# Kernel tuning notes

Hardware: AMD Instinct MI355X
Metric: run time of the kernel (lower is better)

Reference implementation:

```python
import jax, jax.numpy as jnp
import numpy as np

EPS = 1e-05
B, I, N, O = 1024, 256, 1024, 256

def setup_inputs() -> dict:
    key = jax.random.key(0)
    ks = jax.random.split(key, 6)
    return {
        "x_re": jax.random.normal(ks[0], (B, I, 1), dtype=jnp.float32),
        "x_im": jax.random.normal(ks[1], (B, I, 1), dtype=jnp.float32),
        "G_re": jax.random.normal(ks[2], (I, N), dtype=jnp.float32) / np.sqrt(I).astype(np.float32),
        "G_im": jax.random.normal(ks[3], (I, N), dtype=jnp.float32) / np.sqrt(I).astype(np.float32),
        "s_re": jnp.ones((1, N), dtype=jnp.float32),
        "s_im": jnp.ones((1, N), dtype=jnp.float32),
        "W_re": jax.random.normal(ks[4], (N, O), dtype=jnp.float32) * np.float32(np.sqrt(5 * np.exp(2) * I / (12 * N * O))),
        "W_im": jax.random.normal(ks[5], (N, O), dtype=jnp.float32) * np.float32(np.sqrt(5 * np.exp(2) * I / (12 * N * O))),
        "b_re": jnp.zeros((1, O), dtype=jnp.float32),
        "b_im": jnp.zeros((1, O), dtype=jnp.float32),
    }

def reference(x_re, x_im, G_re, G_im, s_re, s_im, W_re, W_im, b_re, b_im):
    # (B, inputs, 1) - (inputs, neurons) -> (B, inputs, neurons); reduce over inputs
    v_re = jnp.sum((x_re - G_re) ** 2, axis=1, keepdims=True)  # (B, 1, N)
    v_im = jnp.sum((x_im - G_im) ** 2, axis=1, keepdims=True)  # (B, 1, N)
    phi_re = jnp.exp(-v_re / jnp.maximum(s_re, EPS))  # (B, 1, N)
    phi_im = jnp.exp(-v_im / jnp.maximum(s_im, EPS))  # (B, 1, N)
    # complex matmul (phi_re + i phi_im) @ (W_re + i W_im) + (b_re + i b_im)
    y_re = jnp.matmul(phi_re, W_re) - jnp.matmul(phi_im, W_im) + b_re  # (B, 1, O)
    y_im = jnp.matmul(phi_re, W_im) + jnp.matmul(phi_im, W_re) + b_im  # (B, 1, O)
    return jnp.stack([y_re, y_im], axis=-1)  # (B, 1, O, 2) = real/imag
```

## Files before the change

### kernel.cpp

```cpp
#include <hip/hip_runtime.h>
#include <math.h>

#define B_ 1024
#define I_ 256
#define N_ 1024
#define O_ 256
#define EPSV 1e-5f

typedef unsigned short u16;
typedef short bf16x8 __attribute__((ext_vector_type(8)));
typedef float f32x4 __attribute__((ext_vector_type(4)));
typedef int i32x4 __attribute__((ext_vector_type(4)));

__device__ inline u16 f2bf(float f) {
    union { float f; unsigned int u; } v; v.f = f;
    unsigned int r = v.u + 0x7FFFu + ((v.u >> 16) & 1u);
    return (u16)(r >> 16);
}


__device__ inline void transconv_frag(const float* __restrict__ in,
                                      u16* __restrict__ out, int R, int C,
                                      int r0, int c0, int t, float (*tile)[69],
                                      float* __restrict__ gpart) {
    const int lr = t >> 2, lq = t & 3;
    #pragma unroll
    for (int j = 0; j < 4; ++j) {
        float4 v = *(const float4*)(in + (size_t)(r0 + lr) * C + c0 + lq * 16 + j * 4);
        *(float4*)&tile[lr][lq * 16 + j * 4] = v;
    }
    __syncthreads();
    const int oc = t >> 2, oq = t & 3;
    const int row = c0 + oc;
    const int ktiles = R >> 5;
    float ss = 0.f;
    #pragma unroll
    for (int h = 0; h < 2; ++h) {
        const int k0 = r0 + oq * 16 + h * 8;
        const int kt = k0 >> 5, quad = (k0 >> 3) & 3;
        __align__(16) u16 tmp[8];
        #pragma unroll
        for (int e = 0; e < 8; ++e) {
            const float g = tile[oq * 16 + h * 8 + e][oc];
            ss += g * g;
            tmp[e] = f2bf(g);
        }
        const size_t off = ((size_t)((row >> 4) * ktiles + kt)) * 512
                         + (quad * 16 + (row & 15)) * 8;
        *(int4*)(out + off) = *(const int4*)tmp;
    }
    if (gpart) {
        ss += __shfl_xor(ss, 1);
        ss += __shfl_xor(ss, 2);
        if (oq == 0) gpart[(r0 >> 6) * C + row] = ss;
    }
}

__global__ __launch_bounds__(256) void prep_kernel(
    const float* __restrict__ x_re, const float* __restrict__ x_im,
    const float* __restrict__ G_re, const float* __restrict__ G_im,
    const float* __restrict__ W_re, const float* __restrict__ W_im,
    u16* __restrict__ Xfr, u16* __restrict__ Xfi,
    u16* __restrict__ GTfr, u16* __restrict__ GTfi,
    u16* __restrict__ WTfr, u16* __restrict__ WTfi,
    float* __restrict__ xsq_re, float* __restrict__ xsq_im,
    float* __restrict__ gsq_re_part, float* __restrict__ gsq_im_part)
{
    __shared__ float smem[64][69];
    const int blk = blockIdx.x, t = threadIdx.x;

    if (blk < 32) {
        const int unit = blk * 4 + (t >> 6);
        const int comp = unit >> 6, mt = unit & 63;
        const int lane = t & 63;
        const int l16 = lane & 15, quad = lane >> 4;
        const float* src = (comp ? x_im : x_re)
                         + (size_t)(mt * 16 + l16) * I_ + quad * 8;
        u16* dstbase = (comp ? Xfi : Xfr) + (size_t)(mt * 8) * 512 + lane * 8;
        float ssum = 0.f;
        #pragma unroll
        for (int kt = 0; kt < 8; ++kt) {
            float4 a0 = *(const float4*)(src + kt * 32);
            float4 a1 = *(const float4*)(src + kt * 32 + 4);
            ssum += a0.x*a0.x + a0.y*a0.y + a0.z*a0.z + a0.w*a0.w
                  + a1.x*a1.x + a1.y*a1.y + a1.z*a1.z + a1.w*a1.w;
            __align__(16) u16 tmp[8];
            tmp[0] = f2bf(a0.x); tmp[1] = f2bf(a0.y);
            tmp[2] = f2bf(a0.z); tmp[3] = f2bf(a0.w);
            tmp[4] = f2bf(a1.x); tmp[5] = f2bf(a1.y);
            tmp[6] = f2bf(a1.z); tmp[7] = f2bf(a1.w);
            *(int4*)(dstbase + (size_t)kt * 512) = *(const int4*)tmp;
        }
        ssum += __shfl_xor(ssum, 16);
        ssum += __shfl_xor(ssum, 32);
        if (lane < 16) {
            float* xsq = comp ? xsq_im : xsq_re;
            xsq[mt * 16 + lane] = ssum;
        }
    } else if (blk < 160) {
        const int local = blk - 32;
        const int comp = local >> 6, rem = local & 63;
        const int rt = rem >> 4, ct = rem & 15;
        transconv_frag(comp ? G_im : G_re, comp ? GTfi : GTfr,
                       I_, N_, rt * 64, ct * 64, t, smem,
                       comp ? gsq_im_part : gsq_re_part);
    } else {
        const int local = blk - 160;
        const int comp = local >> 6, rem = local & 63;
        const int rt = rem >> 2, ct = rem & 3;
        transconv_frag(comp ? W_im : W_re, comp ? WTfi : WTfr,
                       N_, O_, rt * 64, ct * 64, t, smem, (float*)0);
    }
}

__global__ __launch_bounds__(256) void phi_mfma(
    const u16* __restrict__ Xfr, const u16* __restrict__ Xfi,
    const u16* __restrict__ GTfr, const u16* __restrict__ GTfi,
    const float* __restrict__ xsq_re, const float* __restrict__ xsq_im,
    const float* __restrict__ gsq_re_part, const float* __restrict__ gsq_im_part,
    const float* __restrict__ s_re, const float* __restrict__ s_im,
    u16* __restrict__ Pfr, u16* __restrict__ Pfi)
{
    __shared__ u16 pbuf[8 * 512];
    const int z = blockIdx.z;
    const u16* Xf  = z ? Xfi : Xfr;
    const u16* GTf = z ? GTfi : GTfr;
    const float* xsq = z ? xsq_im : xsq_re;
    const float* gp  = z ? gsq_im_part : gsq_re_part;
    const float* s   = z ? s_im : s_re;
    u16* Pf = z ? Pfi : Pfr;

    const int t = threadIdx.x;
    const int w = t >> 6, lane = t & 63;
    const int quad = lane >> 4, l16 = lane & 15;
    const int mw = (w >> 1) * 32, nw = (w & 1) * 32;
    const int mt0 = blockIdx.y * 4 + (mw >> 4);
    const int nt0 = blockIdx.x * 4 + (nw >> 4);

    const u16* Ab = Xf  + lane * 8;
    const u16* Bb = GTf + lane * 8;
    const size_t a0o = (size_t)(mt0 * 8) * 512;
    const size_t a1o = (size_t)((mt0 + 1) * 8) * 512;
    const size_t b0o = (size_t)(nt0 * 8) * 512;
    const size_t b1o = (size_t)((nt0 + 1) * 8) * 512;

    bf16x8 cA0 = *(const bf16x8*)(Ab + a0o);
    bf16x8 cA1 = *(const bf16x8*)(Ab + a1o);
    bf16x8 cB0 = *(const bf16x8*)(Bb + b0o);
    bf16x8 cB1 = *(const bf16x8*)(Bb + b1o);

    f32x4 acc[2][2] = {};
    #pragma unroll
    for (int kt = 0; kt < 8; ++kt) {
        bf16x8 nA0, nA1, nB0, nB1;
        if (kt < 7) {
            const size_t ko = (size_t)(kt + 1) * 512;
            nA0 = *(const bf16x8*)(Ab + a0o + ko);
            nA1 = *(const bf16x8*)(Ab + a1o + ko);
            nB0 = *(const bf16x8*)(Bb + b0o + ko);
            nB1 = *(const bf16x8*)(Bb + b1o + ko);
        }
        acc[0][0] = __builtin_amdgcn_mfma_f32_16x16x32_bf16(cA0, cB0, acc[0][0], 0, 0, 0);
        acc[0][1] = __builtin_amdgcn_mfma_f32_16x16x32_bf16(cA0, cB1, acc[0][1], 0, 0, 0);
        acc[1][0] = __builtin_amdgcn_mfma_f32_16x16x32_bf16(cA1, cB0, acc[1][0], 0, 0, 0);
        acc[1][1] = __builtin_amdgcn_mfma_f32_16x16x32_bf16(cA1, cB1, acc[1][1], 0, 0, 0);
        cA0 = nA0; cA1 = nA1; cB0 = nB0; cB1 = nB1;
    }

    const int m0 = blockIdx.y * 64, n0 = blockIdx.x * 64;
    #pragma unroll
    for (int mt = 0; mt < 2; ++mt)
        #pragma unroll
        for (int nt = 0; nt < 2; ++nt) {
            const int col = nw + nt * 16 + l16;
            const int gn = n0 + col;
            const float gq = gp[gn] + gp[N_ + gn] + gp[2 * N_ + gn] + gp[3 * N_ + gn];
            const float inv_s = 1.0f / fmaxf(s[gn], EPSV);
            #pragma unroll
            for (int r = 0; r < 4; ++r) {
                const int row = mw + mt * 16 + quad * 4 + r;
                const float v = xsq[m0 + row] - 2.0f * acc[mt][nt][r] + gq;
                const u16 p = f2bf(__expf(-v * inv_s));
                const int lt = (row >> 4) * 2 + (col >> 5);
                pbuf[lt * 512 + (((col >> 3) & 3) * 16 + (row & 15)) * 8 + (col & 7)] = p;
            }
        }
    __syncthreads();

    const int lt = t >> 5, s32 = t & 31;
    const int mt_g = blockIdx.y * 4 + (lt >> 1);
    const int kt_g = blockIdx.x * 2 + (lt & 1);
    const u16* src = pbuf + lt * 512 + s32 * 16;
    u16* dst = Pf + (size_t)(mt_g * 32 + kt_g) * 512 + s32 * 16;
    *(int4*)dst = *(const int4*)src;
    *((int4*)dst + 1) = *((const int4*)src + 1);
}

__global__ __launch_bounds__(256) void y_mfma(
    const u16* __restrict__ Pfr, const u16* __restrict__ Pfi,
    const u16* __restrict__ WTfr, const u16* __restrict__ WTfi,
    const float* __restrict__ b_re, const float* __restrict__ b_im,
    float* __restrict__ out)
{
    __shared__ float red[4][2][16][34];
    const int t = threadIdx.x;
    const int w = t >> 6, lane = t & 63;
    const int quad = lane >> 4, l16 = lane & 15;
    const int pm = blockIdx.y;
    const int wo0 = blockIdx.x * 2;

    const u16* Ar = Pfr + lane * 8;
    const u16* Ai = Pfi + lane * 8;
    const u16* Br = WTfr + lane * 8;
    const u16* Bi = WTfi + lane * 8;
    const size_t ao = (size_t)(pm * 32 + w * 8) * 512;
    const size_t b0o = (size_t)(wo0 * 32 + w * 8) * 512;
    const size_t b1o = (size_t)((wo0 + 1) * 32 + w * 8) * 512;

    bf16x8 cAr = *(const bf16x8*)(Ar + ao);
    bf16x8 cAi = *(const bf16x8*)(Ai + ao);
    bf16x8 cBr0 = *(const bf16x8*)(Br + b0o);
    bf16x8 cBi0 = *(const bf16x8*)(Bi + b0o);
    bf16x8 cBr1 = *(const bf16x8*)(Br + b1o);
    bf16x8 cBi1 = *(const bf16x8*)(Bi + b1o);

    f32x4 cr[2] = {}, ci[2] = {};
    #pragma unroll
    for (int ks = 0; ks < 8; ++ks) {
        bf16x8 nAr, nAi, nBr0, nBi0, nBr1, nBi1;
        if (ks < 7) {
            const size_t ko = (size_t)(ks + 1) * 512;
            nAr  = *(const bf16x8*)(Ar + ao + ko);
            nAi  = *(const bf16x8*)(Ai + ao + ko);
            nBr0 = *(const bf16x8*)(Br + b0o + ko);
            nBi0 = *(const bf16x8*)(Bi + b0o + ko);
            nBr1 = *(const bf16x8*)(Br + b1o + ko);
            nBi1 = *(const bf16x8*)(Bi + b1o + ko);
        }
        i32x4 tv = (*(const i32x4*)&cAi) ^ 0x80008000;
        bf16x8 cAn = *(const bf16x8*)&tv;
        cr[0] = __builtin_amdgcn_mfma_f32_16x16x32_bf16(cAr, cBr0, cr[0], 0, 0, 0);
        cr[0] = __builtin_amdgcn_mfma_f32_16x16x32_bf16(cAn, cBi0, cr[0], 0, 0, 0);
        ci[0] = __builtin_amdgcn_mfma_f32_16x16x32_bf16(cAr, cBi0, ci[0], 0, 0, 0);
        ci[0] = __builtin_amdgcn_mfma_f32_16x16x32_bf16(cAi, cBr0, ci[0], 0, 0, 0);
        cr[1] = __builtin_amdgcn_mfma_f32_16x16x32_bf16(cAr, cBr1, cr[1], 0, 0, 0);
        cr[1] = __builtin_amdgcn_mfma_f32_16x16x32_bf16(cAn, cBi1, cr[1], 0, 0, 0);
        ci[1] = __builtin_amdgcn_mfma_f32_16x16x32_bf16(cAr, cBi1, ci[1], 0, 0, 0);
        ci[1] = __builtin_amdgcn_mfma_f32_16x16x32_bf16(cAi, cBr1, ci[1], 0, 0, 0);
        cAr = nAr; cAi = nAi;
        cBr0 = nBr0; cBi0 = nBi0; cBr1 = nBr1; cBi1 = nBi1;
    }

    #pragma unroll
    for (int nt = 0; nt < 2; ++nt) {
        const int o = nt * 16 + l16;
        #pragma unroll
        for (int r = 0; r < 4; ++r) {
            const int b = quad * 4 + r;
            red[w][0][b][o] = cr[nt][r];
            red[w][1][b][o] = ci[nt][r];
        }
    }
    __syncthreads();

    const int b = t >> 4, oq = t & 15;
    const int o = oq * 2;
    const int gb = blockIdx.y * 16 + b;
    const int go = blockIdx.x * 32 + o;
    float r0 = red[0][0][b][o]   + red[1][0][b][o]   + red[2][0][b][o]   + red[3][0][b][o];
    float i0 = red[0][1][b][o]   + red[1][1][b][o]   + red[2][1][b][o]   + red[3][1][b][o];
    float r1 = red[0][0][b][o+1] + red[1][0][b][o+1] + red[2][0][b][o+1] + red[3][0][b][o+1];
    float i1 = red[0][1][b][o+1] + red[1][1][b][o+1] + red[2][1][b][o+1] + red[3][1][b][o+1];
    float4 v;
    v.x = r0 + b_re[go];     v.y = i0 + b_im[go];
    v.z = r1 + b_re[go + 1]; v.w = i1 + b_im[go + 1];
    *(float4*)(out + ((size_t)gb * O_ + go) * 2) = v;
}

extern "C" void kernel_launch(void* const* d_in, const int* in_sizes, int n_in,
                              void* d_out, int out_size, void* d_ws, size_t ws_size,
                              hipStream_t stream) {
    const float* x_re = (const float*)d_in[0];
    const float* x_im = (const float*)d_in[1];
    const float* G_re = (const float*)d_in[2];
    const float* G_im = (const float*)d_in[3];
    const float* s_re = (const float*)d_in[4];
    const float* s_im = (const float*)d_in[5];
    const float* W_re = (const float*)d_in[6];
    const float* W_im = (const float*)d_in[7];
    const float* b_re = (const float*)d_in[8];
    const float* b_im = (const float*)d_in[9];
    float* out = (float*)d_out;

    u16* Xfr  = (u16*)d_ws;
    u16* Xfi  = Xfr  + (size_t)B_ * I_;
    u16* GTfr = Xfi  + (size_t)B_ * I_;
    u16* GTfi = GTfr + (size_t)N_ * I_;
    u16* WTfr = GTfi + (size_t)N_ * I_;
    u16* WTfi = WTfr + (size_t)O_ * N_;
    u16* Pfr  = WTfi + (size_t)O_ * N_;
    u16* Pfi  = Pfr  + (size_t)B_ * N_;
    float* xsq_re = (float*)(Pfi + (size_t)B_ * N_);
    float* xsq_im = xsq_re + B_;
    float* gsq_re_part = xsq_im + B_;
    float* gsq_im_part = gsq_re_part + 4 * N_;

    prep_kernel<<<288, 256, 0, stream>>>(
        x_re, x_im, G_re, G_im, W_re, W_im,
        Xfr, Xfi, GTfr, GTfi, WTfr, WTfi,
        xsq_re, xsq_im, gsq_re_part, gsq_im_part);

    phi_mfma<<<dim3(N_ / 64, B_ / 64, 2), 256, 0, stream>>>(
        Xfr, Xfi, GTfr, GTfi, xsq_re, xsq_im, gsq_re_part, gsq_im_part,
        s_re, s_im, Pfr, Pfi);

    y_mfma<<<dim3(O_ / 32, B_ / 16), 256, 0, stream>>>(
        Pfr, Pfi, WTfr, WTfi, b_re, b_im, out);
}
```

Baseline: 91.26 us.

## Fuse prep conversion into phi kernel, converting X and G on the fly

Removes the separate prep kernel. The phi kernel now loads fp32 X directly, converts it to bf16 in registers with packed convert instructions, and computes row norms inline. Each block transposes and converts its 64-column G slice into LDS fragments and computes the G norms locally. An extra column of blocks converts W for the y kernel. This saves one launch and the workspace round-trip, but each G slice is now redundantly converted by all 16 row-blocks, and fp32 X is reread per column block.

```diff
diff --git a/kernel.cpp b/kernel.cpp
--- a/kernel.cpp
+++ b/kernel.cpp
@@ -18,11 +18,24 @@
     return (u16)(r >> 16);
 }
 
+__device__ inline bf16x8 cvt8(const float4& a, const float4& b) {
+    union { unsigned int u[4]; bf16x8 v; } r;
+    asm("v_cvt_pk_bf16_f32 %0, %1, %2" : "=v"(r.u[0]) : "v"(a.x), "v"(a.y));
+    asm("v_cvt_pk_bf16_f32 %0, %1, %2" : "=v"(r.u[1]) : "v"(a.z), "v"(a.w));
+    asm("v_cvt_pk_bf16_f32 %0, %1, %2" : "=v"(r.u[2]) : "v"(b.x), "v"(b.y));
+    asm("v_cvt_pk_bf16_f32 %0, %1, %2" : "=v"(r.u[3]) : "v"(b.z), "v"(b.w));
+    return r.v;
+}
+
+__device__ inline float ssq8(const float4& a, const float4& b) {
+    return a.x*a.x + a.y*a.y + a.z*a.z + a.w*a.w
+         + b.x*b.x + b.y*b.y + b.z*b.z + b.w*b.w;
+}
+
 
 __device__ inline void transconv_frag(const float* __restrict__ in,
                                       u16* __restrict__ out, int R, int C,
-                                      int r0, int c0, int t, float (*tile)[69],
-                                      float* __restrict__ gpart) {
+                                      int r0, int c0, int t, float (*tile)[69]) {
     const int lr = t >> 2, lq = t & 3;
     #pragma unroll
     for (int j = 0; j < 4; ++j) {
@@ -33,164 +46,158 @@
     const int oc = t >> 2, oq = t & 3;
     const int row = c0 + oc;
     const int ktiles = R >> 5;
-    float ss = 0.f;
     #pragma unroll
     for (int h = 0; h < 2; ++h) {
         const int k0 = r0 + oq * 16 + h * 8;
         const int kt = k0 >> 5, quad = (k0 >> 3) & 3;
         __align__(16) u16 tmp[8];
         #pragma unroll
-        for (int e = 0; e < 8; ++e) {
-            const float g = tile[oq * 16 + h * 8 + e][oc];
-            ss += g * g;
-            tmp[e] = f2bf(g);
-        }
+        for (int e = 0; e < 8; ++e)
+            tmp[e] = f2bf(tile[oq * 16 + h * 8 + e][oc]);
         const size_t off = ((size_t)((row >> 4) * ktiles + kt)) * 512
                          + (quad * 16 + (row & 15)) * 8;
         *(int4*)(out + off) = *(const int4*)tmp;
     }
-    if (gpart) {
-        ss += __shfl_xor(ss, 1);
-        ss += __shfl_xor(ss, 2);
-        if (oq == 0) gpart[(r0 >> 6) * C + row] = ss;
-    }
-}
-
-__global__ __launch_bounds__(256) void prep_kernel(
+}
+
+__global__ __launch_bounds__(256) void phi_fused(
     const float* __restrict__ x_re, const float* __restrict__ x_im,
     const float* __restrict__ G_re, const float* __restrict__ G_im,
     const float* __restrict__ W_re, const float* __restrict__ W_im,
-    u16* __restrict__ Xfr, u16* __restrict__ Xfi,
-    u16* __restrict__ GTfr, u16* __restrict__ GTfi,
+    const float* __restrict__ s_re, const float* __restrict__ s_im,
     u16* __restrict__ WTfr, u16* __restrict__ WTfi,
-    float* __restrict__ xsq_re, float* __restrict__ xsq_im,
-    float* __restrict__ gsq_re_part, float* __restrict__ gsq_im_part)
-{
-    __shared__ float smem[64][69];
-    const int blk = blockIdx.x, t = threadIdx.x;
-
-    if (blk < 32) {
-        const int unit = blk * 4 + (t >> 6);
-        const int comp = unit >> 6, mt = unit & 63;
-        const int lane = t & 63;
-        const int l16 = lane & 15, quad = lane >> 4;
-        const float* src = (comp ? x_im : x_re)
-                         + (size_t)(mt * 16 + l16) * I_ + quad * 8;
-        u16* dstbase = (comp ? Xfi : Xfr) + (size_t)(mt * 8) * 512 + lane * 8;
-        float ssum = 0.f;
-        #pragma unroll
-        for (int kt = 0; kt < 8; ++kt) {
-            float4 a0 = *(const float4*)(src + kt * 32);
-            float4 a1 = *(const float4*)(src + kt * 32 + 4);
-            ssum += a0.x*a0.x + a0.y*a0.y + a0.z*a0.z + a0.w*a0.w
-                  + a1.x*a1.x + a1.y*a1.y + a1.z*a1.z + a1.w*a1.w;
-            __align__(16) u16 tmp[8];
-            tmp[0] = f2bf(a0.x); tmp[1] = f2bf(a0.y);
-            tmp[2] = f2bf(a0.z); tmp[3] = f2bf(a0.w);
-            tmp[4] = f2bf(a1.x); tmp[5] = f2bf(a1.y);
-            tmp[6] = f2bf(a1.z); tmp[7] = f2bf(a1.w);
-            *(int4*)(dstbase + (size_t)kt * 512) = *(const int4*)tmp;
-        }
-        ssum += __shfl_xor(ssum, 16);
-        ssum += __shfl_xor(ssum, 32);
-        if (lane < 16) {
-            float* xsq = comp ? xsq_im : xsq_re;
-            xsq[mt * 16 + lane] = ssum;
-        }
-    } else if (blk < 160) {
-        const int local = blk - 32;
-        const int comp = local >> 6, rem = local & 63;
-        const int rt = rem >> 4, ct = rem & 15;
-        transconv_frag(comp ? G_im : G_re, comp ? GTfi : GTfr,
-                       I_, N_, rt * 64, ct * 64, t, smem,
-                       comp ? gsq_im_part : gsq_re_part);
-    } else {
-        const int local = blk - 160;
-        const int comp = local >> 6, rem = local & 63;
-        const int rt = rem >> 2, ct = rem & 3;
-        transconv_frag(comp ? W_im : W_re, comp ? WTfi : WTfr,
-                       N_, O_, rt * 64, ct * 64, t, smem, (float*)0);
-    }
-}
-
-__global__ __launch_bounds__(256) void phi_mfma(
-    const u16* __restrict__ Xfr, const u16* __restrict__ Xfi,
-    const u16* __restrict__ GTfr, const u16* __restrict__ GTfi,
-    const float* __restrict__ xsq_re, const float* __restrict__ xsq_im,
-    const float* __restrict__ gsq_re_part, const float* __restrict__ gsq_im_part,
-    const float* __restrict__ s_re, const float* __restrict__ s_im,
     u16* __restrict__ Pfr, u16* __restrict__ Pfi)
 {
-    __shared__ u16 pbuf[8 * 512];
+    __shared__ union ShU {
+        float tile[64][69];
+        u16 pbuf[8 * 512];
+    } sh;
+    __shared__ u16 gfrag[4 * 8 * 512];
+    __shared__ float gsq_l[64];
+
+    const int t = threadIdx.x;
     const int z = blockIdx.z;
-    const u16* Xf  = z ? Xfi : Xfr;
-    const u16* GTf = z ? GTfi : GTfr;
-    const float* xsq = z ? xsq_im : xsq_re;
-    const float* gp  = z ? gsq_im_part : gsq_re_part;
-    const float* s   = z ? s_im : s_re;
+    const int bx = blockIdx.x, by = blockIdx.y;
+
+    if (bx == 16) {
+        const float* Wsrc = z ? W_im : W_re;
+        u16* Wdst = z ? WTfi : WTfr;
+        #pragma unroll
+        for (int j = 0; j < 4; ++j) {
+            transconv_frag(Wsrc, Wdst, N_, O_, by * 64, j * 64, t, sh.tile);
+            __syncthreads();
+        }
+        return;
+    }
+
+    const int n0 = bx * 64;
+    const int m0 = by * 64;
+    const float* Gsrc = z ? G_im : G_re;
+    const float* Xsrc = z ? x_im : x_re;
+    const float* s    = z ? s_im : s_re;
     u16* Pf = z ? Pfi : Pfr;
 
-    const int t = threadIdx.x;
+    const int lr = t >> 2, lq = t & 3;
+    float4 ga[4][4];
+    #pragma unroll
+    for (int c = 0; c < 4; ++c)
+        #pragma unroll
+        for (int j = 0; j < 4; ++j)
+            ga[c][j] = *(const float4*)(Gsrc + (size_t)(c * 64 + lr) * N_
+                                        + n0 + lq * 16 + j * 4);
+    float ssg = 0.f;
+    #pragma unroll
+    for (int c = 0; c < 4; ++c) {
+        #pragma unroll
+        for (int j = 0; j < 4; ++j)
+            *(float4*)&sh.tile[lr][lq * 16 + j * 4] = ga[c][j];
+        __syncthreads();
+        #pragma unroll
+        for (int h = 0; h < 2; ++h) {
+            const int klo = lq * 16 + h * 8;
+            const int kt = c * 2 + (klo >> 5);
+            const int quad = (klo >> 3) & 3;
+            __align__(16) u16 tmp[8];
+            #pragma unroll
+            for (int e = 0; e < 8; ++e) {
+                const float g = sh.tile[klo + e][lr];
+                ssg += g * g;
+                tmp[e] = f2bf(g);
+            }
+            *(int4*)&gfrag[((lr >> 4) * 8 + kt) * 512 + (quad * 16 + (lr & 15)) * 8]
+                = *(const int4*)tmp;
+        }
+        __syncthreads();
+    }
+    ssg += __shfl_xor(ssg, 1);
+    ssg += __shfl_xor(ssg, 2);
+    if (lq == 0) gsq_l[lr] = ssg;
+    __syncthreads();
+
     const int w = t >> 6, lane = t & 63;
     const int quad = lane >> 4, l16 = lane & 15;
     const int mw = (w >> 1) * 32, nw = (w & 1) * 32;
-    const int mt0 = blockIdx.y * 4 + (mw >> 4);
-    const int nt0 = blockIdx.x * 4 + (nw >> 4);
-
-    const u16* Ab = Xf  + lane * 8;
-    const u16* Bb = GTf + lane * 8;
-    const size_t a0o = (size_t)(mt0 * 8) * 512;
-    const size_t a1o = (size_t)((mt0 + 1) * 8) * 512;
-    const size_t b0o = (size_t)(nt0 * 8) * 512;
-    const size_t b1o = (size_t)((nt0 + 1) * 8) * 512;
-
-    bf16x8 cA0 = *(const bf16x8*)(Ab + a0o);
-    bf16x8 cA1 = *(const bf16x8*)(Ab + a1o);
-    bf16x8 cB0 = *(const bf16x8*)(Bb + b0o);
-    bf16x8 cB1 = *(const bf16x8*)(Bb + b1o);
+    const int ntl = nw >> 4;
+
+    const float* xr0 = Xsrc + (size_t)(m0 + mw + l16) * I_ + quad * 8;
+    const float* xr1 = xr0 + (size_t)16 * I_;
+    const u16* bp = gfrag + lane * 8;
+
+    float4 cA00 = *(const float4*)(xr0);
+    float4 cA01 = *(const float4*)(xr0 + 4);
+    float4 cA10 = *(const float4*)(xr1);
+    float4 cA11 = *(const float4*)(xr1 + 4);
 
     f32x4 acc[2][2] = {};
+    float ss0 = 0.f, ss1 = 0.f;
     #pragma unroll
     for (int kt = 0; kt < 8; ++kt) {
-        bf16x8 nA0, nA1, nB0, nB1;
+        float4 nA00, nA01, nA10, nA11;
         if (kt < 7) {
-            const size_t ko = (size_t)(kt + 1) * 512;
-            nA0 = *(const bf16x8*)(Ab + a0o + ko);
-            nA1 = *(const bf16x8*)(Ab + a1o + ko);
-            nB0 = *(const bf16x8*)(Bb + b0o + ko);
-            nB1 = *(const bf16x8*)(Bb + b1o + ko);
-        }
-        acc[0][0] = __builtin_amdgcn_mfma_f32_16x16x32_bf16(cA0, cB0, acc[0][0], 0, 0, 0);
-        acc[0][1] = __builtin_amdgcn_mfma_f32_16x16x32_bf16(cA0, cB1, acc[0][1], 0, 0, 0);
-        acc[1][0] = __builtin_amdgcn_mfma_f32_16x16x32_bf16(cA1, cB0, acc[1][0], 0, 0, 0);
-        acc[1][1] = __builtin_amdgcn_mfma_f32_16x16x32_bf16(cA1, cB1, acc[1][1], 0, 0, 0);
-        cA0 = nA0; cA1 = nA1; cB0 = nB0; cB1 = nB1;
-    }
-
-    const int m0 = blockIdx.y * 64, n0 = blockIdx.x * 64;
+            nA00 = *(const float4*)(xr0 + (kt + 1) * 32);
+            nA01 = *(const float4*)(xr0 + (kt + 1) * 32 + 4);
+            nA10 = *(const float4*)(xr1 + (kt + 1) * 32);
+            nA11 = *(const float4*)(xr1 + (kt + 1) * 32 + 4);
+        }
+        bf16x8 fB0 = *(const bf16x8*)(bp + (size_t)((ntl    ) * 8 + kt) * 512);
+        bf16x8 fB1 = *(const bf16x8*)(bp + (size_t)((ntl + 1) * 8 + kt) * 512);
+        bf16x8 fA0 = cvt8(cA00, cA01);
+        bf16x8 fA1 = cvt8(cA10, cA11);
+        ss0 += ssq8(cA00, cA01);
+        ss1 += ssq8(cA10, cA11);
+        acc[0][0] = __builtin_amdgcn_mfma_f32_16x16x32_bf16(fA0, fB0, acc[0][0], 0, 0, 0);
+        acc[0][1] = __builtin_amdgcn_mfma_f32_16x16x32_bf16(fA0, fB1, acc[0][1], 0, 0, 0);
+        acc[1][0] = __builtin_amdgcn_mfma_f32_16x16x32_bf16(fA1, fB0, acc[1][0], 0, 0, 0);
+        acc[1][1] = __builtin_amdgcn_mfma_f32_16x16x32_bf16(fA1, fB1, acc[1][1], 0, 0, 0);
+        cA00 = nA00; cA01 = nA01; cA10 = nA10; cA11 = nA11;
+    }
+    ss0 += __shfl_xor(ss0, 16); ss0 += __shfl_xor(ss0, 32);
+    ss1 += __shfl_xor(ss1, 16); ss1 += __shfl_xor(ss1, 32);
+
     #pragma unroll
     for (int mt = 0; mt < 2; ++mt)
         #pragma unroll
         for (int nt = 0; nt < 2; ++nt) {
             const int col = nw + nt * 16 + l16;
             const int gn = n0 + col;
-            const float gq = gp[gn] + gp[N_ + gn] + gp[2 * N_ + gn] + gp[3 * N_ + gn];
+            const float gq = gsq_l[col];
             const float inv_s = 1.0f / fmaxf(s[gn], EPSV);
             #pragma unroll
             for (int r = 0; r < 4; ++r) {
                 const int row = mw + mt * 16 + quad * 4 + r;
-                const float v = xsq[m0 + row] - 2.0f * acc[mt][nt][r] + gq;
+                const float xq = __shfl(mt ? ss1 : ss0, quad * 4 + r);
+                const float v = xq - 2.0f * acc[mt][nt][r] + gq;
                 const u16 p = f2bf(__expf(-v * inv_s));
                 const int lt = (row >> 4) * 2 + (col >> 5);
-                pbuf[lt * 512 + (((col >> 3) & 3) * 16 + (row & 15)) * 8 + (col & 7)] = p;
+                sh.pbuf[lt * 512 + (((col >> 3) & 3) * 16 + (row & 15)) * 8 + (col & 7)] = p;
             }
         }
     __syncthreads();
 
-    const int lt = t >> 5, s32 = t & 31;
-    const int mt_g = blockIdx.y * 4 + (lt >> 1);
-    const int kt_g = blockIdx.x * 2 + (lt & 1);
-    const u16* src = pbuf + lt * 512 + s32 * 16;
+    const int lt2 = t >> 5, s32 = t & 31;
+    const int mt_g = by * 4 + (lt2 >> 1);
+    const int kt_g = bx * 2 + (lt2 & 1);
+    const u16* src = sh.pbuf + lt2 * 512 + s32 * 16;
     u16* dst = Pf + (size_t)(mt_g * 32 + kt_g) * 512 + s32 * 16;
     *(int4*)dst = *(const int4*)src;
     *((int4*)dst + 1) = *((const int4*)src + 1);
@@ -292,27 +299,14 @@
     const float* b_im = (const float*)d_in[9];
     float* out = (float*)d_out;
 
-    u16* Xfr  = (u16*)d_ws;
-    u16* Xfi  = Xfr  + (size_t)B_ * I_;
-    u16* GTfr = Xfi  + (size_t)B_ * I_;
-    u16* GTfi = GTfr + (size_t)N_ * I_;
-    u16* WTfr = GTfi + (size_t)N_ * I_;
+    u16* WTfr = (u16*)d_ws;
     u16* WTfi = WTfr + (size_t)O_ * N_;
     u16* Pfr  = WTfi + (size_t)O_ * N_;
     u16* Pfi  = Pfr  + (size_t)B_ * N_;
-    float* xsq_re = (float*)(Pfi + (size_t)B_ * N_);
-    float* xsq_im = xsq_re + B_;
-    float* gsq_re_part = xsq_im + B_;
-    float* gsq_im_part = gsq_re_part + 4 * N_;
-
-    prep_kernel<<<288, 256, 0, stream>>>(
-        x_re, x_im, G_re, G_im, W_re, W_im,
-        Xfr, Xfi, GTfr, GTfi, WTfr, WTfi,
-        xsq_re, xsq_im, gsq_re_part, gsq_im_part);
-
-    phi_mfma<<<dim3(N_ / 64, B_ / 64, 2), 256, 0, stream>>>(
-        Xfr, Xfi, GTfr, GTfi, xsq_re, xsq_im, gsq_re_part, gsq_im_part,
-        s_re, s_im, Pfr, Pfi);
+
+    phi_fused<<<dim3(17, 16, 2), 256, 0, stream>>>(
+        x_re, x_im, G_re, G_im, W_re, W_im, s_re, s_im,
+        WTfr, WTfi, Pfr, Pfi);
 
     y_mfma<<<dim3(O_ / 32, B_ / 16), 256, 0, stream>>>(
         Pfr, Pfi, WTfr, WTfi, b_re, b_im, out);
```

Result: slower. 111.5 us (+22.2%).
